# Kernel optimization log

Measured on AMD Instinct MI355X. Metric: run time of the kernel, lower is better.

Reference implementation:

```python
import jax, jax.numpy as jnp
import numpy as np

B, N, C_IN, C_EMB, G = 16, 1024, 16, 64, 128
NEG = -1e12


def _lap(m):
    # m @ D^-1/2, transpose, @ D^-1/2  (matches torch code incl. transpose)
    d = jnp.sum(m, axis=1) ** -0.5
    return (m * d[None, :]).T * d[None, :]


def setup_inputs():
    key = jax.random.key(0)
    ks = jax.random.split(key, 16)
    f = jax.random.normal
    return {
        'x': f(ks[0], (B, C_IN, N), jnp.float32),
        'ct': f(ks[1], (B, C_EMB, N), jnp.float32),
        'graph_data': jax.random.uniform(ks[2], (2, N, N), dtype=jnp.float32),
        'emb_w': f(ks[3], (C_EMB, C_IN)) / np.sqrt(C_IN).astype(np.float32),
        'emb_b': f(ks[4], (C_EMB,)) * 0.01,
        'emb2_w': f(ks[5], (N, N)) / np.sqrt(N).astype(np.float32),
        'emb2_b': f(ks[6], (N,)) * 0.01,
        'att_W': f(ks[7], (C_EMB, C_EMB)) / np.sqrt(C_EMB).astype(np.float32),
        'att_a': f(ks[8], (2 * C_EMB, 1)) / np.sqrt(2 * C_EMB).astype(np.float32),
        'att_GL': f(ks[9], (N, G)) / np.sqrt(G).astype(np.float32),
        'uai_w': f(ks[10], (C_EMB, C_EMB)) / np.sqrt(C_EMB).astype(np.float32),
        'uai_b': f(ks[11], (C_EMB,)) * 0.01,
        'lin1_w': f(ks[12], (C_EMB, C_EMB)) / np.sqrt(C_EMB).astype(np.float32),
        'lin2_w': f(ks[13], (C_EMB, C_EMB)) / np.sqrt(C_EMB).astype(np.float32),
        'lin2_b': f(ks[14], (C_EMB,)) * 0.01,
        'ln_w': jnp.ones((C_EMB, N), jnp.float32),
        'ln_b': jnp.zeros((C_EMB, N), jnp.float32),
    }


def reference(x, ct, graph_data, emb_w, emb_b, emb2_w, emb2_b, att_W, att_a,
              att_GL, uai_w, uai_b, lin1_w, lin2_w, lin2_b, ln_w, ln_b):
    # emb: Conv1d k=1 -> leaky_relu -> Linear over node axis N
    h0 = jax.nn.leaky_relu(jnp.einsum('bcn,ec->ben', x, emb_w) + emb_b[None, :, None])
    h0 = jnp.einsum('ben,mn->bem', h0, emb2_w) + emb2_b[None, None, :]
    inp = jnp.swapaxes(h0, 1, 2)  # [B,N,C']

    # InterpositionAttention (repeat/cat factorized: e_ij = leakyrelu(a1.h_i + a2.h_j))
    eye = jnp.eye(N, dtype=x.dtype)
    adj_att = jax.nn.softmax(jax.nn.relu(att_GL @ att_GL.T), axis=-1) + eye
    h = inp @ att_W  # [B,N,C']
    e = jax.nn.leaky_relu((h @ att_a[:C_EMB]) + jnp.swapaxes(h @ att_a[C_EMB:], 1, 2))  # [B,N,N]
    att = jax.nn.softmax(jnp.where(adj_att > 0, e, NEG), axis=2)
    x_att = jnp.swapaxes(jax.nn.relu(att @ h), 1, 2)  # [B,C',N]

    # UAI module (eval mode: dropout off -> all MC samples equal -> sigma = 0)
    mu = jnp.swapaxes(x_att, 1, 2) @ uai_w.T + uai_b  # [B,N,C']
    x_uai = jnp.swapaxes(mu, 1, 2)  # [B,C',N]

    g1 = _lap(graph_data[0] + eye)
    g2 = _lap(graph_data[1] + eye)

    # learned adjacency from pairwise squared distances (cdist p=2, squared)
    xf = jnp.swapaxes(x_uai, 1, 2)  # [B,N,C']
    sq = jnp.sum(xf * xf, axis=-1)
    d2 = jnp.maximum(sq[:, :, None] + sq[:, None, :] - 2.0 * (xf @ jnp.swapaxes(xf, 1, 2)), 0.0)
    gl = jax.nn.softmax(jnp.exp(-d2 / (2.0 * C_EMB)) + eye, axis=-1)  # sigma^2 = emb_size

    def ln(z):  # LayerNorm over last two dims [C', N]
        m = jnp.mean(z, axis=(1, 2), keepdims=True)
        v = jnp.var(z, axis=(1, 2), keepdims=True)
        return (z - m) / jnp.sqrt(v + 1e-5) * ln_w + ln_b

    l1 = lambda z: jnp.einsum('oc,bcn->bon', lin1_w, z)
    l2 = lambda z: jnp.einsum('oc,bcn->bon', lin2_w, z) + lin2_b[None, :, None]

    x_new = ln(l1(x_uai) @ gl + l1(l1(x_uai) @ g1) @ g2)
    ft = jax.nn.gelu(ln(l2(x_uai) @ gl + l2(l2(x_uai) @ g1) @ g2), approximate=False)
    rt = ft  # rt is computed by the identical expression (dropout off)

    ct_new = ft * ct + x_new - ft * x_new
    ht = rt * jax.nn.elu(ct_new) + x_uai - rt * x_uai
    return (ht, ct_new)
```

## Files before the change

kernel.cpp:

```cpp
#include <hip/hip_runtime.h>
#include <math.h>

typedef unsigned short u16;
typedef __attribute__((ext_vector_type(8))) short short8;
typedef __attribute__((ext_vector_type(4))) float floatx4;

constexpr int BATCH = 16;
constexpr int NI = 1024;
constexpr int CE = 64;
constexpr int CI = 16;
constexpr long long NN2  = (long long)NI * NI;
constexpr long long BCN  = (long long)BATCH * CE * NI;
constexpr long long BNv  = (long long)BATCH * NI;
constexpr long long BNN  = (long long)BATCH * NI * NI;
constexpr long long S1 = (long long)CE * NI;
constexpr long long S2 = 2 * S1;
constexpr int ZERON = (int)(2 * BNv + 80);

__device__ __forceinline__ float lrelu01(float x) { return x > 0.f ? x : 0.01f * x; }

__device__ __forceinline__ u16 f2bf(float f) {
  unsigned u = __builtin_bit_cast(unsigned, f);
  return (u16)((u + 0x7fffu + ((u >> 16) & 1u)) >> 16);
}
__device__ __forceinline__ float bf2f(u16 h) {
  unsigned u = ((unsigned)h) << 16;
  return __builtin_bit_cast(float, u);
}
__device__ __forceinline__ unsigned fkey(float f) {
  unsigned u = __builtin_bit_cast(unsigned, f);
  return (u & 0x80000000u) ? ~u : (u | 0x80000000u);
}
__device__ __forceinline__ float funkey(unsigned k) {
  unsigned u = (k & 0x80000000u) ? (k & 0x7fffffffu) : ~k;
  return __builtin_bit_cast(float, u);
}

__device__ __forceinline__ void gload16(const u16* g, u16* l) {
  __builtin_amdgcn_global_load_lds(
      (const __attribute__((address_space(1))) void*)g,
      (__attribute__((address_space(3))) void*)l, 16, 0, 0);
}

__device__ __forceinline__ void pipe_fence() {
  asm volatile("s_waitcnt vmcnt(0) lgkmcnt(0)" ::: "memory");
  __builtin_amdgcn_sched_barrier(0);
  __builtin_amdgcn_s_barrier();
  __builtin_amdgcn_sched_barrier(0);
}

template<int BM, int BN, int MODE>
__global__ __launch_bounds__(256) void mgemm(
    const u16* __restrict__ Ag, const u16* __restrict__ B1g, const u16* __restrict__ B2g,
    int K1, int K, int lda, int ldb, long long bsA, long long bsB1,
    float* __restrict__ Cf, u16* __restrict__ Cb, int ldc, long long bsC,
    const float* __restrict__ aux1, const float* __restrict__ aux2,
    const float* __restrict__ aux3, const float* __restrict__ aux4,
    float* __restrict__ Zout)
{
  constexpr int RM = BM / 2, RN = BN / 2, MI = RM / 16, NJ = RN / 16;
  constexpr bool PIPE = (MODE == 5 || MODE == 13 || MODE == 14 || MODE == 15);
  constexpr int NBUF = PIPE ? 2 : 1;
  constexpr int NLA = (BM * 8) / 256;
  constexpr int NLB = (BN * 8) / 256;
  __shared__ __align__(16) u16 As[NBUF * BM * 64];
  __shared__ __align__(16) u16 Bs[NBUF * BN * 64];
  __shared__ __align__(16) u16 xa[MODE == 13 ? 32 * 72 : 1];
  const int tid = threadIdx.x;
  int z, n0, r0;
  if constexpr (MODE == 15) {
    const int id = blockIdx.x;
    if (id >= 512) {
      const int m = id - 512;
      float s = 0.f, sv = 0.f;
      for (int n = tid; n < NI; n += 256) {
        float g = aux3[(long long)m * NI + n] * aux2[n];
        s += g;
        sv = fmaf(g, aux1[n], sv);
      }
      float* r1 = (float*)As;
      float* r2 = (float*)As + 256;
      r1[tid] = s; r2[tid] = sv; __syncthreads();
      for (int st = 128; st > 0; st >>= 1) {
        if (tid < st) { r1[tid] += r1[tid + st]; r2[tid] += r2[tid + st]; }
        __syncthreads();
      }
      if (tid == 0) {
        float dm = aux2[m];
        Cf[m] = dm * (r1[0] + dm);
        Zout[m] = dm * (r2[0] + dm * aux1[m]);
      }
      return;
    }
    z = 0; n0 = (id & 15) * BN; r0 = (id >> 4) * BM;
  } else {
    z = blockIdx.z; n0 = blockIdx.x * BN; r0 = blockIdx.y * BM;
  }
  const u16* Ab = Ag + (long long)z * bsA + (long long)r0 * lda;
  const u16* Bb1 = B1g + (long long)z * bsB1 + (long long)n0 * ldb;
  const int lane = tid & 63;
  const int wid = tid >> 6;
  const int wr = wid >> 1, wc = wid & 1;
  const int q = lane >> 4, mlow = lane & 15;
  const int wbase = tid & ~63;

  floatx4 acc[MI][NJ] = {};
  float zp0 = 0.f;

  float s1r_13 = 0.f, mr_13 = 0.f;
  const float* s2z_13 = nullptr;
  if constexpr (MODE == 13) {
    const float* s1z = aux2 + (long long)z * NI;
    s2z_13 = aux3 + (long long)z * NI;
    const float mb = funkey(((const unsigned*)aux4)[z]);
    s1r_13 = s1z[r0 + (tid >> 3)];
    mr_13 = lrelu01(s1r_13 + mb);
  }

  auto stageAB = [&](int buf, int k0) {
    if constexpr (MODE != 13) {
      const u16* Asrc = Ab + k0;
#pragma unroll
      for (int s = 0; s < NLA; s++) {
        int cid = tid + s * 256;
        int r = cid >> 3, cc = cid & 7;
        gload16(Asrc + (long long)r * lda + ((cc ^ (r & 7)) << 3),
                As + buf * (BM * 64) + ((wbase + s * 256) << 3));
      }
    }
    const u16* Bsrc = (k0 < K1) ? (Bb1 + k0)
                                : (B2g + (long long)n0 * ldb + (k0 - K1));
#pragma unroll
    for (int s = 0; s < NLB; s++) {
      int cid = tid + s * 256;
      int r = cid >> 3, cc = cid & 7;
      gload16(Bsrc + (long long)r * ldb + ((cc ^ (r & 7)) << 3),
              Bs + buf * (BN * 64) + ((wbase + s * 256) << 3));
    }
  };

  auto agen = [&](int buf, int k0) {
    int r = tid >> 3, craw = tid & 7;
    const float* sp = s2z_13 + k0 + craw * 8;
    float4 sa = *(const float4*)sp;
    float4 sb = *(const float4*)(sp + 4);
    float p0 = __expf(lrelu01(s1r_13 + sa.x) - mr_13);
    float p1 = __expf(lrelu01(s1r_13 + sa.y) - mr_13);
    float p2 = __expf(lrelu01(s1r_13 + sa.z) - mr_13);
    float p3 = __expf(lrelu01(s1r_13 + sa.w) - mr_13);
    float p4 = __expf(lrelu01(s1r_13 + sb.x) - mr_13);
    float p5 = __expf(lrelu01(s1r_13 + sb.y) - mr_13);
    float p6 = __expf(lrelu01(s1r_13 + sb.z) - mr_13);
    float p7 = __expf(lrelu01(s1r_13 + sb.w) - mr_13);
    zp0 += p0 + p1 + p2 + p3 + p4 + p5 + p6 + p7;
    uint4 v;
    v.x = (unsigned)f2bf(p0) | ((unsigned)f2bf(p1) << 16);
    v.y = (unsigned)f2bf(p2) | ((unsigned)f2bf(p3) << 16);
    v.z = (unsigned)f2bf(p4) | ((unsigned)f2bf(p5) << 16);
    v.w = (unsigned)f2bf(p6) | ((unsigned)f2bf(p7) << 16);
    *(uint4*)&As[buf * (BM * 64) + (r * 8 + (craw ^ (r & 7))) * 8] = v;
  };

  auto compute_tile = [&](int buf) {
#pragma unroll
    for (int kh = 0; kh < 2; kh++) {
      const int kc = kh * 4 + q;
      short8 afr[MI], bfr[NJ];
#pragma unroll
      for (int i = 0; i < MI; i++) {
        int row = wr * RM + i * 16 + mlow;
        afr[i] = *(const short8*)&As[buf * (BM * 64) + (row * 8 + (kc ^ (row & 7))) * 8];
      }
#pragma unroll
      for (int j = 0; j < NJ; j++) {
        int row = wc * RN + j * 16 + mlow;
        bfr[j] = *(const short8*)&Bs[buf * (BN * 64) + (row * 8 + (kc ^ (row & 7))) * 8];
      }
#pragma unroll
      for (int i = 0; i < MI; i++)
#pragma unroll
        for (int j = 0; j < NJ; j++)
          acc[i][j] = __builtin_amdgcn_mfma_f32_16x16x32_bf16(afr[i], bfr[j], acc[i][j], 0, 0, 0);
    }
  };

  if constexpr (PIPE) {
    stageAB(0, 0);
    if constexpr (MODE == 13) agen(0, 0);
    pipe_fence();
    int cur = 0;
    for (int k0 = 0; k0 < K; k0 += 64) {
      if (k0 + 64 < K) {
        stageAB(cur ^ 1, k0 + 64);
        if constexpr (MODE == 13) agen(cur ^ 1, k0 + 64);
      }
      compute_tile(cur);
      pipe_fence();
      cur ^= 1;
    }
  } else {
    for (int k0 = 0; k0 < K; k0 += 64) {
      stageAB(0, k0);
      __syncthreads();
      compute_tile(0);
      __syncthreads();
    }
  }

  if constexpr (MODE == 3) {
    const float* sqb = aux1 + (long long)z * NI;
#pragma unroll
    for (int i = 0; i < MI; i++) {
#pragma unroll
      for (int rg = 0; rg < 4; rg++) {
        int r = r0 + wr * RM + i * 16 + q * 4 + rg;
        float sqi = sqb[r];
        float rsum = 0.f;
#pragma unroll
        for (int j = 0; j < NJ; j++) {
          int ncol = n0 + wc * RN + j * 16 + mlow;
          float d2 = fmaxf(sqi + sqb[ncol] - 2.f * acc[i][j][rg], 0.f);
          float w = __expf(__expf(-d2 * (1.f / 128.f)) + (r == ncol ? 1.f : 0.f) - 2.f);
          Cb[(long long)z * bsC + (long long)r * ldc + ncol] = f2bf(w);
          rsum += w;
        }
        rsum += __shfl_xor(rsum, 1);
        rsum += __shfl_xor(rsum, 2);
        rsum += __shfl_xor(rsum, 4);
        rsum += __shfl_xor(rsum, 8);
        if (mlow == 0) atomicAdd(&Zout[(long long)z * NI + r], rsum);
      }
    }
  } else if constexpr (MODE == 14) {
    float ps1 = 0.f, ps2 = 0.f;
#pragma unroll
    for (int i = 0; i < MI; i++) {
#pragma unroll
      for (int rg = 0; rg < 4; rg++) {
        int r = wr * RM + i * 16 + q * 4 + rg;
        int ncol = n0 + wc * RN + mlow;
        float v = acc[i][0][rg] + aux3[r] * aux1[ncol];
        Cb[(long long)z * bsC + (long long)r * ldc + ncol] = f2bf(v);
        ps1 = fmaf(v, aux2[r], ps1);
        ps2 = fmaf(v, aux2[64 + r], ps2);
      }
    }
    ps1 += __shfl_xor(ps1, 16); ps1 += __shfl_xor(ps1, 32);
    ps2 += __shfl_xor(ps2, 16); ps2 += __shfl_xor(ps2, 32);
    float* sred = (float*)As;
    const int col = wc * RN + mlow;
    if (q == 0) { sred[col * 2 + wr] = ps1; sred[64 + col * 2 + wr] = ps2; }
    __syncthreads();
    if (tid < 32) {
      float v1 = sred[tid * 2] + sred[tid * 2 + 1];
      float v2 = sred[64 + tid * 2] + sred[64 + tid * 2 + 1];
      Cf[(long long)z * NI + n0 + tid] = v1;
      Zout[(long long)z * NI + n0 + tid] = v2;
      float mx = v2;
      for (int off = 1; off < 32; off <<= 1) mx = fmaxf(mx, __shfl_xor(mx, off));
      if (tid == 0) atomicMax((unsigned*)B2g + z, fkey(mx));
    }
  } else if constexpr (MODE == 13) {
    float* zred = (float*)xa;
    float* zinv = (float*)xa + 256;
    zred[(tid >> 3) * 8 + (tid & 7)] = zp0;
    __syncthreads();
    if (tid < 32) {
      float sum = 0.f;
#pragma unroll
      for (int j = 0; j < 8; j++) sum += zred[tid * 8 + j];
      zinv[tid] = 1.f / sum;
    }
    __syncthreads();
    float zr[4];
#pragma unroll
    for (int rg = 0; rg < 4; rg++) zr[rg] = zinv[wr * 16 + q * 4 + rg];
    __syncthreads();
#pragma unroll
    for (int j = 0; j < NJ; j++) {
#pragma unroll
      for (int rg = 0; rg < 4; rg++) {
        int row = wr * 16 + q * 4 + rg;
        int col = wc * RN + j * 16 + mlow;
        float v = fmaxf(acc[0][j][rg] * zr[rg], 0.f);
        xa[row * 72 + col] = f2bf(v);
      }
    }
#pragma unroll
    for (int s = 0; s < 2; s++) {
      int cid = tid + s * 256;
      int r = cid >> 3, cc = cid & 7;
      gload16(B2g + r * 64 + ((cc ^ (r & 7)) << 3),
              Bs + ((wbase + s * 256) << 3));
    }
    __syncthreads();
    floatx4 acc2[2] = {};
#pragma unroll
    for (int kh = 0; kh < 2; kh++) {
      const int kc = kh * 4 + q;
      short8 a2 = *(const short8*)&xa[(wr * 16 + mlow) * 72 + kc * 8];
#pragma unroll
      for (int j = 0; j < 2; j++) {
        int orow = wc * 32 + j * 16 + mlow;
        short8 b2 = *(const short8*)&Bs[(orow * 8 + (kc ^ (orow & 7))) * 8];
        acc2[j] = __builtin_amdgcn_mfma_f32_16x16x32_bf16(a2, b2, acc2[j], 0, 0, 0);
      }
    }
#pragma unroll
    for (int rg = 0; rg < 4; rg++) {
      int row = r0 + wr * 16 + q * 4 + rg;
      float sqp = 0.f;
#pragma unroll
      for (int j = 0; j < 2; j++) {
        int o = wc * 32 + j * 16 + mlow;
        float v = acc2[j][rg] + aux1[o];
        Cb[(long long)z * bsC + (long long)row * ldc + o] = f2bf(v);
        sqp = fmaf(v, v, sqp);
      }
      sqp += __shfl_xor(sqp, 1);
      sqp += __shfl_xor(sqp, 2);
      sqp += __shfl_xor(sqp, 4);
      sqp += __shfl_xor(sqp, 8);
      if (mlow == 0) atomicAdd(&Zout[(long long)z * NI + row], sqp);
    }
  } else if constexpr (MODE == 5) {
    float ts = 0.f, tss = 0.f;
#pragma unroll
    for (int i = 0; i < MI; i++) {
#pragma unroll
      for (int j = 0; j < NJ; j++) {
#pragma unroll
        for (int rg = 0; rg < 4; rg++) {
          int r = r0 + wr * RM + i * 16 + q * 4 + rg;
          int ncol = n0 + wc * RN + j * 16 + mlow;
          float v = acc[i][j][rg];
          v += aux3[r] * aux1[ncol] + aux4[r] * aux2[ncol];
          Cb[(long long)z * bsC + (long long)r * ldc + ncol] = f2bf(v);
          ts += v;
          tss = fmaf(v, v, tss);
        }
      }
    }
    float* red = (float*)As;
    red[tid] = ts; red[256 + tid] = tss;
    __syncthreads();
    for (int st = 128; st > 0; st >>= 1) {
      if (tid < st) { red[tid] += red[tid + st]; red[256 + tid] += red[256 + tid + st]; }
      __syncthreads();
    }
    if (tid == 0) {
      const int half = r0 >> 6;
      atomicAdd(&Zout[z * 2 + half], red[0]);
      atomicAdd(&Zout[32 + z * 2 + half], red[256]);
    }
  } else {
#pragma unroll
    for (int i = 0; i < MI; i++) {
#pragma unroll
      for (int j = 0; j < NJ; j++) {
#pragma unroll
        for (int rg = 0; rg < 4; rg++) {
          int r = r0 + wr * RM + i * 16 + q * 4 + rg;
          int ncol = n0 + wc * RN + j * 16 + mlow;
          float v = acc[i][j][rg];
          if constexpr (MODE == 4) {
            int blk = r >> 6, oo = r & 63;
            int drow = ((blk & 1) << 6) + oo;
            if (blk < 2) v = (v + aux3[drow]) / aux1[(long long)z * NI + ncol];
            Cb[(long long)z * bsC + (long long)drow * 2048 + (long long)(blk >> 1) * 1024 + ncol] =
                f2bf(v);
          } else {
            Cb[(long long)z * bsC + (long long)r * ldc + ncol] = f2bf(v);
          }
        }
      }
    }
  }
}

__global__ __launch_bounds__(256) void lap_rowsum(const float* __restrict__ gd,
                                                  float* __restrict__ dr,
                                                  float* __restrict__ zero)
{
  if (blockIdx.x >= 2048) {
    int i = (blockIdx.x - 2048) * 256 + threadIdx.x;
    if (i < ZERON) zero[i] = 0.f;
    return;
  }
  const int ki = blockIdx.x;
  const float* row = gd + (long long)ki * NI;
  float s = 0.f;
  for (int j = threadIdx.x; j < NI; j += 256) s += row[j];
  __shared__ float red[256];
  red[threadIdx.x] = s; __syncthreads();
  for (int st = 128; st > 0; st >>= 1) {
    if (threadIdx.x < st) red[threadIdx.x] += red[threadIdx.x + st];
    __syncthreads();
  }
  if (threadIdx.x == 0) dr[ki] = rsqrtf(red[0] + 1.f);
}

__global__ __launch_bounds__(256) void mega_prep(
    const float* __restrict__ l1w, const float* __restrict__ l2w,
    const float* __restrict__ l2b, const float* __restrict__ uaiw,
    const float* __restrict__ attW,
    u16* __restrict__ stack4, float* __restrict__ rb2ext, float* __restrict__ rl2ext,
    u16* __restrict__ uaiw_bf, u16* __restrict__ attwT_bf, float* __restrict__ wcs,
    const float* __restrict__ emb2w, u16* __restrict__ emb2w_bf,
    const float* __restrict__ x, const float* __restrict__ ew,
    const float* __restrict__ eb, u16* __restrict__ h0aT,
    const float* __restrict__ gd, const float* __restrict__ dsum,
    u16* __restrict__ g2t, u16* __restrict__ g1,
    float* __restrict__ cs1)
{
  __shared__ float sm[1092];
  const int bid = blockIdx.x;
  const int t = threadIdx.x;
  if (bid < 98) {
    const int gid = bid * 256 + t;
    if (gid < 4096) {
      stack4[gid] = f2bf(l1w[gid]);
    } else if (gid < 8192) {
      stack4[gid] = f2bf(l2w[gid - 4096]);
    } else if (gid < 12288) {
      int tt = gid - 8192, o = tt >> 6, m = tt & 63;
      float s = 0.f;
      for (int c = 0; c < 64; c++) s = fmaf(l1w[o * 64 + c], l1w[c * 64 + m], s);
      stack4[gid] = f2bf(s);
    } else if (gid < 16384) {
      int tt = gid - 12288, o = tt >> 6, m = tt & 63;
      float s = 0.f;
      for (int c = 0; c < 64; c++) s = fmaf(l2w[o * 64 + c], l2w[c * 64 + m], s);
      stack4[gid] = f2bf(s);
    } else if (gid < 16512) {
      int r = gid - 16384;
      rb2ext[r] = (r < 64) ? 0.f : l2b[r - 64];
    } else if (gid < 16640) {
      int r = gid - 16512;
      float v = 0.f;
      if (r >= 64) { int o = r - 64; for (int c = 0; c < 64; c++) v = fmaf(l2w[o * 64 + c], l2b[c], v); }
      rl2ext[r] = v;
    } else if (gid < 20736) {
      uaiw_bf[gid - 16640] = f2bf(uaiw[gid - 16640]);
    } else if (gid < 24832) {
      int idx = gid - 20736;
      int c = idx >> 6, e = idx & 63;
      attwT_bf[idx] = f2bf(attW[e * 64 + c]);
    } else if (gid < 24896) {
      int c = gid - 24832;
      float s = 0.f;
      for (int e = 0; e < 64; e++) s += attW[e * 64 + c];
      wcs[c] = s;
    }
  } else if (bid < 4194) {
    const long long i = (long long)(bid - 98) * 256 + t;
    emb2w_bf[i] = f2bf(emb2w[i]);
  } else if (bid < 4450) {
    const int sub = bid - 4194;
    const int b = sub >> 4;
    const int nc = (sub & 15) * 64;
    float* we = sm;
    float* be = sm + 1024;
    for (int i = t; i < 1024; i += 256) we[i] = ew[i];
    if (t < 64) be[t] = eb[t];
    __syncthreads();
    const int n = nc + (t >> 2);
    const int e0 = (t & 3) * 16;
    const float* xb = x + (long long)b * CI * NI + n;
    float xv[16];
#pragma unroll
    for (int c = 0; c < CI; c++) xv[c] = xb[(long long)c * NI];
    u16 out16[16];
#pragma unroll
    for (int ee = 0; ee < 16; ee++) {
      const int e = e0 + ee;
      float a = be[e];
#pragma unroll
      for (int c = 0; c < CI; c++) a = fmaf(xv[c], we[e * 16 + c], a);
      out16[ee] = f2bf(lrelu01(a));
    }
    u16* dst = h0aT + (long long)b * S1 + (long long)n * 64 + e0;
    *(uint4*)dst = *(uint4*)out16;
    *(uint4*)(dst + 8) = *(uint4*)(out16 + 8);
  } else if (bid < 8546) {
    const long long idx = (long long)(bid - 4450) * 256 + t;
    const int m = (int)(idx >> 10), j = (int)(idx & 1023);
    const float* d = dsum + NI;
    float v = (gd[NN2 + idx] + (m == j ? 1.f : 0.f)) * d[m] * d[j];
    g2t[idx] = f2bf(v);
  } else if (bid < 9570) {
    const int sub = bid - 8546;
    const int bx = (sub & 31) * 32, by = (sub >> 5) * 32;
    const int lx = t & 31, ly = t >> 5;
    float* tile = sm;
    for (int yy = ly; yy < 32; yy += 8)
      tile[yy * 33 + lx] = gd[(long long)(by + yy) * NI + bx + lx];
    __syncthreads();
    for (int yy = ly; yy < 32; yy += 8) {
      const int i = bx + yy, j = by + lx;
      float v = (tile[lx * 33 + yy] + (i == j ? 1.f : 0.f)) * dsum[i] * dsum[j];
      g1[(long long)i * NI + j] = f2bf(v);
    }
  } else {
    const int n = bid - 9570;
    float s = 0.f;
    for (int i = t; i < NI; i += 256) s = fmaf(gd[(long long)n * NI + i], dsum[i], s);
    float* red = sm;
    red[t] = s; __syncthreads();
    for (int st = 128; st > 0; st >>= 1) {
      if (t < st) red[t] += red[t + st];
      __syncthreads();
    }
    if (t == 0) cs1[n] = dsum[n] * (red[0] + dsum[n]);
  }
}

__global__ __launch_bounds__(256) void ln_final_t(const u16* __restrict__ T,
                                                  const float* __restrict__ stats,
                                                  const float* __restrict__ lnw,
                                                  const float* __restrict__ lnb,
                                                  const float* __restrict__ ct,
                                                  const u16* __restrict__ xuT,
                                                  float* __restrict__ outp)
{
  __shared__ float xs[64 * 65];
  const int blk = blockIdx.x;
  const int b = blk >> 4;
  const int n0 = (blk & 15) << 6;
  const int t = threadIdx.x;
  const int tc = t & 63, tr = t >> 6;
#pragma unroll
  for (int i = 0; i < 16; i++) {
    int nn = i * 4 + tr;
    xs[tc * 65 + nn] = bf2f(xuT[((long long)b << 16) + (long long)(n0 + nn) * 64 + tc]);
  }
  __syncthreads();
  const float inv_n = 1.f / 65536.f;
  const float m0 = stats[b * 2] * inv_n;
  const float m1 = stats[b * 2 + 1] * inv_n;
  const float rs0 = rsqrtf(fmaxf(stats[32 + b * 2] * inv_n - m0 * m0, 0.f) + 1e-5f);
  const float rs1 = rsqrtf(fmaxf(stats[32 + b * 2 + 1] * inv_n - m1 * m1, 0.f) + 1e-5f);
#pragma unroll
  for (int j = 0; j < 16; j++) {
    const int c = j * 4 + tr;
    const int n = n0 + tc;
    const int rem = c * NI + n;
    const long long toff = (long long)b * S2 + rem;
    const float t0 = bf2f(T[toff]);
    const float t1 = bf2f(T[toff + S1]);
    const float w = lnw[rem], bb = lnb[rem];
    const float xn = (t0 - m0) * rs0 * w + bb;
    float ft = (t1 - m1) * rs1 * w + bb;
    ft = 0.5f * ft * (1.f + erff(ft * 0.70710678118654752f));
    const float u = xs[c * 65 + tc];
    const long long oidx = ((long long)b << 16) + rem;
    const float cn = fmaf(ft, ct[oidx] - xn, xn);
    const float el = cn > 0.f ? cn : expm1f(cn);
    outp[oidx] = fmaf(ft, el - u, u);
    outp[BCN + oidx] = cn;
  }
}

extern "C" void kernel_launch(void* const* d_in, const int* in_sizes, int n_in,
                              void* d_out, int out_size, void* d_ws, size_t ws_size,
                              hipStream_t stream)
{
  (void)in_sizes; (void)n_in; (void)out_size; (void)ws_size;
  const float* x      = (const float*)d_in[0];
  const float* ct     = (const float*)d_in[1];
  const float* gdata  = (const float*)d_in[2];
  const float* emb_w  = (const float*)d_in[3];
  const float* emb_b  = (const float*)d_in[4];
  const float* emb2_w = (const float*)d_in[5];
  const float* emb2_b = (const float*)d_in[6];
  const float* att_W  = (const float*)d_in[7];
  const float* att_a  = (const float*)d_in[8];
  const float* uai_w  = (const float*)d_in[10];
  const float* uai_b  = (const float*)d_in[11];
  const float* lin1_w = (const float*)d_in[12];
  const float* lin2_w = (const float*)d_in[13];
  const float* lin2_b = (const float*)d_in[14];
  const float* ln_w   = (const float*)d_in[15];
  const float* ln_b   = (const float*)d_in[16];
  float* outp = (float*)d_out;

  float* ws = (float*)d_ws;
  long long o = 0;
  auto af = [&](long long n) { float* p = ws + o; o += (n + 63) & ~63LL; return p; };
  auto au = [&](long long n) { return (u16*)af((n + 1) / 2); };

  float* s1      = af(BNv);
  float* s2      = af(BNv);
  float* dsum    = af(2 * NI);
  float* cs1v    = af(NI);
  float* cs2v    = af(NI);
  float* v2v     = af(NI);
  float* rb2ext  = af(128);
  float* rl2ext  = af(128);
  float* wcs     = af(64);
  float* zeroreg = af(ZERON);
  float* Zgl     = zeroreg;
  float* sqv     = zeroreg + BNv;
  float* stats   = zeroreg + 2 * BNv;
  unsigned* s2mU = (unsigned*)(stats + 64);
  u16* Tacc      = au(S2 * BATCH);
  u16* emb2w_bf  = au(NN2);
  u16* h0aTb     = au(S1 * BATCH);
  u16* ybf       = au(S1 * BATCH);
  u16* hTb       = au(S1 * BATCH);
  u16* xuaiTb    = au(S1 * BATCH);
  u16* g1b       = au(NN2);
  u16* g2tb      = au(NN2);
  u16* G12b      = au(NN2);
  u16* Abig      = au((long long)BATCH * 128 * 2048);
  u16* stack4    = au(256 * 64);
  u16* uaiw_bf   = au(CE * CE);
  u16* attwT_bf  = au(CE * CE);
  u16* bigW      = au(BNN);

  lap_rowsum<<<2048 + (ZERON + 255) / 256, 256, 0, stream>>>(gdata, dsum, zeroreg);

  mega_prep<<<10594, 256, 0, stream>>>(
      lin1_w, lin2_w, lin2_b, uai_w, att_W,
      stack4, rb2ext, rl2ext, uaiw_bf, attwT_bf, wcs,
      emb2_w, emb2w_bf, x, emb_w, emb_b, h0aTb,
      gdata, dsum, g2tb, g1b, cs1v);

  mgemm<32, 64, 15><<<1536, 256, 0, stream>>>(
      g2tb, g1b, nullptr, NI, NI, NI, NI, 0, 0,
      cs2v, G12b, NI, 0, cs1v, dsum + NI, gdata + NN2, nullptr, v2v);

  mgemm<64, 64, 6><<<dim3(16, 1, BATCH), 256, 0, stream>>>(
      attwT_bf, h0aTb, nullptr, CE, CE, CE, CE, 0, S1,
      nullptr, ybf, NI, S1, nullptr, nullptr, nullptr, nullptr, nullptr);

  mgemm<64, 32, 14><<<dim3(32, 1, BATCH), 256, 0, stream>>>(
      ybf, emb2w_bf, (const u16*)s2mU, NI, NI, NI, NI, S1, 0,
      s1, hTb, NI, S1, emb2_b, att_a, wcs, nullptr, s2);

  mgemm<32, 64, 13><<<dim3(1, 32, BATCH), 256, 0, stream>>>(
      hTb, hTb, uaiw_bf, NI, NI, NI, NI, 0, S1,
      nullptr, xuaiTb, CE, S1, uai_b, s1, s2, (const float*)s2mU, sqv);

  mgemm<128, 128, 3><<<dim3(8, 8, BATCH), 256, 0, stream>>>(
      xuaiTb, xuaiTb, nullptr, CE, CE, CE, CE, S1, S1,
      nullptr, bigW, NI, NN2, sqv, nullptr, nullptr, nullptr, Zgl);

  mgemm<64, 64, 4><<<dim3(16, 4, BATCH), 256, 0, stream>>>(
      stack4, xuaiTb, nullptr, CE, CE, CE, CE, 0, S1,
      nullptr, Abig, 0, (long long)128 * 2048, Zgl, nullptr, rb2ext, nullptr, nullptr);

  mgemm<64, 64, 5><<<dim3(16, 2, BATCH), 256, 0, stream>>>(
      Abig, bigW, G12b, NI, 2 * NI, 2048, NI, (long long)128 * 2048, NN2,
      nullptr, Tacc, NI, S2, cs2v, v2v, rb2ext, rl2ext, stats);

  ln_final_t<<<256, 256, 0, stream>>>(Tacc, stats, ln_w, ln_b, ct, xuaiTb, outp);
}
```

Before: 232.4 us.

## Deepen GEMM prefetch pipeline to multi-stage buffers with partial vmcnt waits

The pipelined GEMM modes (5, 14, 15) move from double buffering to a 3-stage ring, or 4 stages for mode 5. Waits use s_waitcnt vmcnt with counts of outstanding loads instead of a full drain, so later tiles' loads can stay in flight while the current tile is computed. Mode 13 splits its softmax-score generation so the global reads are issued before the async staging. The mode-6 GEMM uses narrower tiles across more blocks, and the final LN kernel runs 512 threads per block. The cost is more LDS per block, which may lower occupancy, and correctness now depends on the per-thread load counts being exact.

```diff
diff --git a/kernel.cpp b/kernel.cpp
--- a/kernel.cpp
+++ b/kernel.cpp
@@ -49,6 +49,21 @@
   __builtin_amdgcn_sched_barrier(0);
 }
 
+template<int N>
+__device__ __forceinline__ void fence_bar() {
+  __builtin_amdgcn_sched_barrier(0);
+  if constexpr (N == 0) asm volatile("s_waitcnt vmcnt(0)" ::: "memory");
+  else if constexpr (N == 1) asm volatile("s_waitcnt vmcnt(1)" ::: "memory");
+  else if constexpr (N == 2) asm volatile("s_waitcnt vmcnt(2)" ::: "memory");
+  else if constexpr (N == 3) asm volatile("s_waitcnt vmcnt(3)" ::: "memory");
+  else if constexpr (N == 4) asm volatile("s_waitcnt vmcnt(4)" ::: "memory");
+  else if constexpr (N == 6) asm volatile("s_waitcnt vmcnt(6)" ::: "memory");
+  else if constexpr (N == 8) asm volatile("s_waitcnt vmcnt(8)" ::: "memory");
+  else asm volatile("s_waitcnt vmcnt(0)" ::: "memory");
+  __builtin_amdgcn_s_barrier();
+  __builtin_amdgcn_sched_barrier(0);
+}
+
 template<int BM, int BN, int MODE>
 __global__ __launch_bounds__(256) void mgemm(
     const u16* __restrict__ Ag, const u16* __restrict__ B1g, const u16* __restrict__ B2g,
@@ -59,10 +74,12 @@
     float* __restrict__ Zout)
 {
   constexpr int RM = BM / 2, RN = BN / 2, MI = RM / 16, NJ = RN / 16;
-  constexpr bool PIPE = (MODE == 5 || MODE == 13 || MODE == 14 || MODE == 15);
-  constexpr int NBUF = PIPE ? 2 : 1;
+  constexpr bool PIPE3 = (MODE == 5 || MODE == 14 || MODE == 15);
+  constexpr int DEPTH = (MODE == 5) ? 4 : 3;
+  constexpr int NBUF = PIPE3 ? DEPTH : (MODE == 13 ? 2 : 1);
   constexpr int NLA = (BM * 8) / 256;
   constexpr int NLB = (BN * 8) / 256;
+  constexpr int L = (MODE == 13) ? NLB : (NLA + NLB);
   __shared__ __align__(16) u16 As[NBUF * BM * 64];
   __shared__ __align__(16) u16 Bs[NBUF * BN * 64];
   __shared__ __align__(16) u16 xa[MODE == 13 ? 32 * 72 : 1];
@@ -109,6 +126,7 @@
 
   float s1r_13 = 0.f, mr_13 = 0.f;
   const float* s2z_13 = nullptr;
+  float4 sa, sb;
   if constexpr (MODE == 13) {
     const float* s1z = aux2 + (long long)z * NI;
     s2z_13 = aux3 + (long long)z * NI;
@@ -139,11 +157,13 @@
     }
   };
 
-  auto agen = [&](int buf, int k0) {
+  auto agen_ld = [&](int k0) {
+    const float* sp = s2z_13 + k0 + (tid & 7) * 8;
+    sa = *(const float4*)sp;
+    sb = *(const float4*)(sp + 4);
+  };
+  auto agen_st = [&](int buf) {
     int r = tid >> 3, craw = tid & 7;
-    const float* sp = s2z_13 + k0 + craw * 8;
-    float4 sa = *(const float4*)sp;
-    float4 sb = *(const float4*)(sp + 4);
     float p0 = __expf(lrelu01(s1r_13 + sa.x) - mr_13);
     float p1 = __expf(lrelu01(s1r_13 + sa.y) - mr_13);
     float p2 = __expf(lrelu01(s1r_13 + sa.z) - mr_13);
@@ -184,15 +204,42 @@
     }
   };
 
-  if constexpr (PIPE) {
+  if constexpr (PIPE3) {
+    const int nk = K >> 6;
+#pragma unroll
+    for (int p = 0; p < DEPTH - 1; p++) stageAB(p, p << 6);
+    fence_bar<(DEPTH - 2) * L>();
+    int cur = 0, stg = DEPTH - 1;
+    for (int ki = 0; ki < nk; ki++) {
+      if (ki + DEPTH - 1 < nk) stageAB(stg, (ki + DEPTH - 1) << 6);
+      compute_tile(cur);
+      if (ki + 1 < nk) {
+        const int rem = nk - 1 - ki;
+        const int u = (rem < DEPTH - 1) ? rem : (DEPTH - 1);
+        if constexpr (DEPTH == 4) {
+          if (u == 3) fence_bar<2 * L>();
+          else if (u == 2) fence_bar<L>();
+          else fence_bar<0>();
+        } else {
+          if (u == 2) fence_bar<L>();
+          else fence_bar<0>();
+        }
+      }
+      cur++; if (cur == NBUF) cur = 0;
+      stg++; if (stg == NBUF) stg = 0;
+    }
+    __syncthreads();
+  } else if constexpr (MODE == 13) {
+    agen_ld(0);
     stageAB(0, 0);
-    if constexpr (MODE == 13) agen(0, 0);
+    agen_st(0);
     pipe_fence();
     int cur = 0;
     for (int k0 = 0; k0 < K; k0 += 64) {
       if (k0 + 64 < K) {
+        agen_ld(k0 + 64);
         stageAB(cur ^ 1, k0 + 64);
-        if constexpr (MODE == 13) agen(cur ^ 1, k0 + 64);
+        agen_st(cur ^ 1);
       }
       compute_tile(cur);
       pipe_fence();
@@ -515,7 +562,7 @@
   }
 }
 
-__global__ __launch_bounds__(256) void ln_final_t(const u16* __restrict__ T,
+__global__ __launch_bounds__(512) void ln_final_t(const u16* __restrict__ T,
                                                   const float* __restrict__ stats,
                                                   const float* __restrict__ lnw,
                                                   const float* __restrict__ lnb,
@@ -530,8 +577,8 @@
   const int t = threadIdx.x;
   const int tc = t & 63, tr = t >> 6;
 #pragma unroll
-  for (int i = 0; i < 16; i++) {
-    int nn = i * 4 + tr;
+  for (int i = 0; i < 8; i++) {
+    int nn = i * 8 + tr;
     xs[tc * 65 + nn] = bf2f(xuT[((long long)b << 16) + (long long)(n0 + nn) * 64 + tc]);
   }
   __syncthreads();
@@ -541,8 +588,8 @@
   const float rs0 = rsqrtf(fmaxf(stats[32 + b * 2] * inv_n - m0 * m0, 0.f) + 1e-5f);
   const float rs1 = rsqrtf(fmaxf(stats[32 + b * 2 + 1] * inv_n - m1 * m1, 0.f) + 1e-5f);
 #pragma unroll
-  for (int j = 0; j < 16; j++) {
-    const int c = j * 4 + tr;
+  for (int j = 0; j < 8; j++) {
+    const int c = j * 8 + tr;
     const int n = n0 + tc;
     const int rem = c * NI + n;
     const long long toff = (long long)b * S2 + rem;
@@ -630,7 +677,7 @@
       g2tb, g1b, nullptr, NI, NI, NI, NI, 0, 0,
       cs2v, G12b, NI, 0, cs1v, dsum + NI, gdata + NN2, nullptr, v2v);
 
-  mgemm<64, 64, 6><<<dim3(16, 1, BATCH), 256, 0, stream>>>(
+  mgemm<64, 32, 6><<<dim3(32, 1, BATCH), 256, 0, stream>>>(
       attwT_bf, h0aTb, nullptr, CE, CE, CE, CE, 0, S1,
       nullptr, ybf, NI, S1, nullptr, nullptr, nullptr, nullptr, nullptr);
 
@@ -654,5 +701,5 @@
       Abig, bigW, G12b, NI, 2 * NI, 2048, NI, (long long)128 * 2048, NN2,
       nullptr, Tacc, NI, S2, cs2v, v2v, rb2ext, rl2ext, stats);
 
-  ln_final_t<<<256, 256, 0, stream>>>(Tacc, stats, ln_w, ln_b, ct, xuaiTb, outp);
-}
+  ln_final_t<<<256, 512, 0, stream>>>(Tacc, stats, ln_w, ln_b, ct, xuaiTb, outp);
+}
```

Result: no change. 229.6 us (-1.2%).
